# Kernel optimization log

Hardware: AMD Instinct MI355X
Metric: run time of the kernel (lower is better)

## Reference

```python
import jax, jax.numpy as jnp
import numpy as np
import math

D_MODEL = 1024
N_HEADS = 16
D_K = D_MODEL // N_HEADS


def setup_inputs() -> dict:
    key = jax.random.key(0)
    ks = jax.random.split(key, 5)
    std = math.sqrt(2.0 / (D_MODEL + D_MODEL))
    x = jax.random.normal(ks[0], (2, 2048, D_MODEL), dtype=jnp.float32)
    W_q = jax.random.normal(ks[1], (D_MODEL, D_MODEL), dtype=jnp.float32) * std
    W_k = jax.random.normal(ks[2], (D_MODEL, D_MODEL), dtype=jnp.float32) * std
    W_v = jax.random.normal(ks[3], (D_MODEL, D_MODEL), dtype=jnp.float32) * std
    W_o = jax.random.normal(ks[4], (D_MODEL, D_MODEL), dtype=jnp.float32) * std
    return {"x": x, "W_q": W_q, "W_k": W_k, "W_v": W_v, "W_o": W_o}


def reference(x, W_q, W_k, W_v, W_o):
    B, S, D = x.shape
    H, dk = N_HEADS, D_K
    # projections: (B,S,D) @ (D,D)
    def split_heads(t):  # (B,S,D) -> (B,H,S,dk)
        return t.reshape(B, S, H, dk).transpose(0, 2, 1, 3)
    Q = split_heads(x @ W_q)
    K = split_heads(x @ W_k)
    V = split_heads(x @ W_v)
    scale = 1.0 / math.sqrt(dk)
    scores = jnp.einsum("bhqd,bhkd->bhqk", Q, K) * scale  # (B,H,S,S)
    attn = jax.nn.softmax(scores, axis=-1)
    out = jnp.einsum("bhqk,bhkd->bhqd", attn, V)  # (B,H,S,dk)
    concat = out.transpose(0, 2, 1, 3).reshape(B, S, D)
    return concat @ W_o
```

## Files before the change

### kernel.cpp

```cpp
#include <hip/hip_runtime.h>
#include <hip/hip_bf16.h>
#include <math.h>

#define DMODEL 1024
#define NHEADS 16
#define DKH    64
#define BATCH  2
#define SEQ    2048
#define MROWS  (BATCH * SEQ)
#define LOG2E  1.4426950408889634f

typedef __bf16 bf16_t;
typedef bf16_t bf16x8 __attribute__((ext_vector_type(8)));
typedef bf16_t bf16x4 __attribute__((ext_vector_type(4)));
typedef float  floatx4 __attribute__((ext_vector_type(4)));

__device__ __forceinline__ void glds16(const bf16_t* g, bf16_t* l) {
    __builtin_amdgcn_global_load_lds((__attribute__((address_space(1))) unsigned*)(g),
                                     (__attribute__((address_space(3))) unsigned*)(l),
                                     16, 0, 0);
}

__global__ void prep_kernel(const float* __restrict__ x,
                            const float* __restrict__ W0, const float* __restrict__ W1,
                            const float* __restrict__ W2, const float* __restrict__ W3,
                            bf16_t* __restrict__ xb, bf16_t* __restrict__ Wt) {
    __shared__ float t[32][33];
    int bx = blockIdx.x, by = blockIdx.y, z = blockIdx.z;
    int tx = threadIdx.x, ty = threadIdx.y;
    if (z == 0) {
        int tid = ty * 32 + tx;
#pragma unroll
        for (int k = 0; k < 4; ++k) {
            int slot = k * 256 + tid;
            int row = by * 128 + (slot >> 3);
            int col = bx * 32 + (slot & 7) * 4;
            float4 v = *(const float4*)&x[(size_t)row * DMODEL + col];
            bf16x4 o = {(bf16_t)v.x, (bf16_t)v.y, (bf16_t)v.z, (bf16_t)v.w};
            *(bf16x4*)&xb[(size_t)row * DMODEL + col] = o;
        }
        return;
    }
    const float* W = (z == 1) ? W0 : (z == 2) ? W1 : (z == 3) ? W2 : W3;
    bf16_t* dst = Wt + (size_t)(z - 1) * DMODEL * DMODEL;
#pragma unroll
    for (int i = 0; i < 32; i += 8)
        t[ty + i][tx] = W[(size_t)(by * 32 + ty + i) * DMODEL + bx * 32 + tx];
    __syncthreads();
#pragma unroll
    for (int i = 0; i < 32; i += 8)
        dst[(size_t)(bx * 32 + ty + i) * DMODEL + by * 32 + tx] = (bf16_t)t[tx][ty + i];
}

__global__ __launch_bounds__(512) void gemm_qkv_kernel(const bf16_t* __restrict__ A,
                                                       const bf16_t* __restrict__ Bt,
                                                       bf16_t* __restrict__ Qfb,
                                                       bf16_t* __restrict__ Kfb,
                                                       bf16_t* __restrict__ Vfb) {
    extern __shared__ __align__(16) bf16_t sm[];
    int tid = threadIdx.x;
    int w = tid >> 6, l = tid & 63, g = l >> 4, lm = l & 15;
    int wr = w >> 2, wc = w & 3;
    int m0 = blockIdx.y * 256, n0 = blockIdx.x * 256;

    int w8l3 = w * 8 + (l >> 3);
    int cw8  = ((l & 7) ^ (l >> 3)) * 8;
    const bf16_t* Ag0 = A  + (size_t)m0 * DMODEL;
    const bf16_t* Bg0 = Bt + (size_t)n0 * DMODEL;

#define STAGE(MATB, LDSB, hh, tt) do {                                             \
        const bf16_t* _src = (MATB) + (size_t)((hh) * 128 + w8l3) * DMODEL + (tt) * 64 + cw8; \
        bf16_t* _dst = (LDSB) + (hh) * 8192 + w * 8 * 64;                          \
        glds16(_src, _dst);                                                        \
        glds16(_src + (size_t)64 * DMODEL, _dst + 4096);                           \
    } while (0)

#define PH_SYNC() do { asm volatile("s_waitcnt vmcnt(4)" ::: "memory");            \
        __builtin_amdgcn_s_barrier(); __builtin_amdgcn_sched_barrier(0); } while (0)
#define PH_BAR() do { __builtin_amdgcn_s_barrier();                                \
        __builtin_amdgcn_sched_barrier(0); } while (0)

    floatx4 a00[4][2], a01[4][2], a10[4][2], a11[4][2];
#pragma unroll
    for (int i = 0; i < 4; ++i)
#pragma unroll
        for (int j = 0; j < 2; ++j) {
            floatx4 z = {0.f, 0.f, 0.f, 0.f};
            a00[i][j] = z; a01[i][j] = z; a10[i][j] = z; a11[i][j] = z;
        }
    bf16x8 af[4][2], bf0[2][2], bf1[2][2];

#define LOAD_AF(ihh, bb) do {                                                      \
        const bf16_t* _ab = sm + (bb) * 16384 + (ihh) * 8192;                      \
        _Pragma("unroll")                                                          \
        for (int i = 0; i < 4; ++i) {                                              \
            int _hr = (wr * 64 + i * 16 + lm) * 64;                                \
            af[i][0] = *(const bf16x8*)&_ab[_hr + ((g) ^ (lm & 7)) * 8];           \
            af[i][1] = *(const bf16x8*)&_ab[_hr + ((4 + g) ^ (lm & 7)) * 8];       \
        } } while (0)

#define LOAD_BF(BF, jhh, bb) do {                                                  \
        const bf16_t* _bb = sm + 32768 + (bb) * 16384 + (jhh) * 8192;              \
        _Pragma("unroll")                                                          \
        for (int j = 0; j < 2; ++j) {                                              \
            int _bc = (wc * 32 + j * 16 + lm) * 64;                                \
            BF[j][0] = *(const bf16x8*)&_bb[_bc + ((g) ^ (lm & 7)) * 8];           \
            BF[j][1] = *(const bf16x8*)&_bb[_bc + ((4 + g) ^ (lm & 7)) * 8];       \
        } } while (0)

#define MM(ACC, BF) do {                                                           \
        __builtin_amdgcn_s_setprio(1);                                             \
        _Pragma("unroll")                                                          \
        for (int kk = 0; kk < 2; ++kk)                                             \
        _Pragma("unroll")                                                          \
        for (int i = 0; i < 4; ++i)                                                \
        _Pragma("unroll")                                                          \
        for (int j = 0; j < 2; ++j)                                                \
            ACC[i][j] = __builtin_amdgcn_mfma_f32_16x16x32_bf16(af[i][kk], BF[j][kk], ACC[i][j], 0, 0, 0); \
        __builtin_amdgcn_s_setprio(0);                                             \
    } while (0)

    STAGE(Ag0, sm, 0, 0);
    STAGE(Bg0, sm + 32768, 0, 0);
    STAGE(Bg0, sm + 32768, 1, 0);
    STAGE(Ag0, sm, 1, 0);

    for (int t = 0; t < 16; ++t) {
        int buf = t & 1;
        bf16_t* An = sm + (buf ^ 1) * 16384;
        bf16_t* Bn = sm + 32768 + (buf ^ 1) * 16384;
        int tn = (t + 1) & 15;

        PH_SYNC();
        STAGE(Ag0, An, 0, tn);
        LOAD_AF(0, buf);
        LOAD_BF(bf0, 0, buf);
        MM(a00, bf0);
        PH_SYNC();
        STAGE(Bg0, Bn, 0, tn);
        LOAD_BF(bf1, 1, buf);
        MM(a01, bf1);
        PH_SYNC();
        STAGE(Bg0, Bn, 1, tn);
        LOAD_AF(1, buf);
        MM(a11, bf1);
        PH_BAR();
        STAGE(Ag0, An, 1, tn);
        MM(a10, bf0);
    }

    __syncthreads();
    int mat = blockIdx.x >> 2;
    int headb = (blockIdx.x & 3) * 4;
    int b = m0 >> 11;
    int ktb = (m0 & 2047) >> 6;
    const float scaleQ = 0.125f * LOG2E;

#define EPI(ACC, ihh, jhh)                                                          \
    _Pragma("unroll")                                                               \
    for (int i = 0; i < 4; ++i)                                                     \
    _Pragma("unroll")                                                               \
    for (int j = 0; j < 2; ++j) {                                                   \
        int s0_ = (ihh) * 128 + wr * 64 + i * 16 + g * 4;                           \
        int d_  = (jhh) * 128 + wc * 32 + j * 16 + lm;                              \
        int hc_ = d_ >> 6, d6 = d_ & 63, st_ = s0_ >> 6, s6 = s0_ & 63;             \
        int chunk = hc_ * 4 + st_;                                                  \
        if (mat == 0) {                                                             \
            int base = chunk * 4096 + ((s6 >> 4) * 2 + (d6 >> 5)) * 512 +           \
                       ((d6 >> 3) & 3) * 128 + (s6 & 15) * 8 + (d6 & 7);            \
            _Pragma("unroll")                                                       \
            for (int r = 0; r < 4; ++r)                                             \
                sm[base + r * 8] = (bf16_t)(ACC[i][j][r] * scaleQ);                 \
        } else if (mat == 1) {                                                      \
            int base = chunk * 4096 + (((s6 >> 5) & 1) * 4 + ((s6 >> 2) & 1) * 2 + (d6 >> 5)) * 512 + \
                       ((d6 >> 3) & 3) * 128 +                                      \
                       (((s6 >> 4) & 1) * 8 + ((s6 >> 3) & 1) * 4) * 8 + (d6 & 7);  \
            _Pragma("unroll")                                                       \
            for (int r = 0; r < 4; ++r)                                             \
                sm[base + r * 8] = (bf16_t)ACC[i][j][r];                            \
        } else {                                                                    \
            int base = chunk * 4096 + ((d6 >> 4) * 2 + ((s6 >> 5) & 1)) * 512 +     \
                       ((((s6 >> 4) & 1) * 2 + ((s6 >> 3) & 1)) * 16 + (d6 & 15)) * 8 + \
                       ((s6 >> 2) & 1) * 4;                                         \
            bf16x4 pk = {(bf16_t)ACC[i][j][0], (bf16_t)ACC[i][j][1],                \
                         (bf16_t)ACC[i][j][2], (bf16_t)ACC[i][j][3]};               \
            *(bf16x4*)&sm[base] = pk;                                               \
        }                                                                           \
    }

    EPI(a00, 0, 0);
    EPI(a01, 0, 1);
    EPI(a10, 1, 0);
    EPI(a11, 1, 1);

    __syncthreads();
    bf16_t* outbuf = (mat == 0) ? Qfb : (mat == 1) ? Kfb : Vfb;
#pragma unroll
    for (int rep = 0; rep < 16; ++rep) {
        int idx = rep * 512 + tid;
        int c = idx >> 9;
        int off = (idx & 511) * 8;
        int bh2 = b * NHEADS + headb + (c >> 2);
        int kt = ktb + (c & 3);
        *(bf16x8*)(outbuf + ((size_t)bh2 * 32 + kt) * 4096 + off) = *(const bf16x8*)&sm[c * 4096 + off];
    }
#undef STAGE
#undef PH_SYNC
#undef PH_BAR
#undef LOAD_AF
#undef LOAD_BF
#undef MM
#undef EPI
}

__global__ __launch_bounds__(256) void gemmO_kernel(const bf16_t* __restrict__ A,
                                                    const bf16_t* __restrict__ Bt,
                                                    float* __restrict__ outp) {
    __shared__ bf16_t As[64 * 64];
    __shared__ bf16_t Bs[128 * 64];
    int tid = threadIdx.x;
    int w = tid >> 6, l = tid & 63, g = l >> 4, lm = l & 15;
    int wr = w & 1, wc = w >> 1;
    int m0 = blockIdx.y * 64, n0 = blockIdx.x * 128;
    int r8 = l >> 3, s8 = l & 7, cw = s8 ^ r8;

    floatx4 acc[2][4];
#pragma unroll
    for (int i = 0; i < 2; ++i)
#pragma unroll
        for (int j = 0; j < 4; ++j) { floatx4 z = {0.f, 0.f, 0.f, 0.f}; acc[i][j] = z; }

    const bf16_t* Ag = A  + (size_t)(m0 + w * 16 + r8) * DMODEL + cw * 8;
    const bf16_t* Bg = Bt + (size_t)(n0 + w * 32 + r8) * DMODEL + cw * 8;

    for (int k0 = 0; k0 < DMODEL; k0 += 64) {
        __syncthreads();
#pragma unroll
        for (int j = 0; j < 2; ++j)
            glds16(Ag + (size_t)j * 8 * DMODEL + k0, &As[(w * 16 + j * 8) * 64]);
#pragma unroll
        for (int j = 0; j < 4; ++j)
            glds16(Bg + (size_t)j * 8 * DMODEL + k0, &Bs[(w * 32 + j * 8) * 64]);
        __syncthreads();
#pragma unroll
        for (int kk = 0; kk < 2; ++kk) {
            bf16x8 af[2], bfr[4];
            int c = kk * 4 + g;
            int sw = (c ^ (lm & 7)) * 8;
#pragma unroll
            for (int i = 0; i < 2; ++i)
                af[i] = *(const bf16x8*)&As[(wr * 32 + i * 16 + lm) * 64 + sw];
#pragma unroll
            for (int j = 0; j < 4; ++j)
                bfr[j] = *(const bf16x8*)&Bs[(wc * 64 + j * 16 + lm) * 64 + sw];
#pragma unroll
            for (int i = 0; i < 2; ++i)
#pragma unroll
                for (int j = 0; j < 4; ++j)
                    acc[i][j] = __builtin_amdgcn_mfma_f32_16x16x32_bf16(af[i], bfr[j], acc[i][j], 0, 0, 0);
        }
    }

#pragma unroll
    for (int i = 0; i < 2; ++i)
#pragma unroll
        for (int j = 0; j < 4; ++j) {
            int nc = n0 + wc * 64 + j * 16 + lm;
            int mb = m0 + wr * 32 + i * 16 + g * 4;
#pragma unroll
            for (int r = 0; r < 4; ++r)
                outp[(size_t)(mb + r) * DMODEL + nc] = acc[i][j][r];
        }
}

__global__ __launch_bounds__(256, 2) void attn_kernel(const bf16_t* __restrict__ Qf,
                                                      const bf16_t* __restrict__ Kf,
                                                      const bf16_t* __restrict__ Vf,
                                                      bf16_t* __restrict__ Cc) {
    __shared__ __align__(16) char smem[24576];
    float*  Mbuf = (float*)smem;
    float*  Lbuf = (float*)(smem + 20480);
    bf16_t* Ct   = (bf16_t*)(smem + 21504);

    int tid = threadIdx.x;
    int w = tid >> 6, l = tid & 63, g = l >> 4, lm = l & 15;
    int bh = blockIdx.x, b = bh >> 4, h = bh & 15;
    int q0 = blockIdx.y * 64;

    const bf16_t* Qfh = Qf + ((size_t)bh * 32 + (q0 >> 6)) * 4096 + l * 8;
    const bf16_t* Kfh = Kf + (size_t)bh * 32 * 4096 + l * 8;
    const bf16_t* Vfh = Vf + (size_t)bh * 32 * 4096 + l * 8;

    bf16x8 qf[4][2];
#pragma unroll
    for (int nt = 0; nt < 4; ++nt)
#pragma unroll
        for (int kk = 0; kk < 2; ++kk)
            qf[nt][kk] = *(const bf16x8*)(Qfh + (nt * 2 + kk) * 512);

    floatx4 oacc[4][4];
#pragma unroll
    for (int dt = 0; dt < 4; ++dt)
#pragma unroll
        for (int nt = 0; nt < 4; ++nt) { floatx4 z = {0.f, 0.f, 0.f, 0.f}; oacc[dt][nt] = z; }
    float lsum[4] = {0.f, 0.f, 0.f, 0.f};

    int kt0 = w * 8;
    bf16x8 kfa[2][2], kfb[2][2], vfa[4], vfb[4];
    {
        const bf16_t* Kb0 = Kfh + (size_t)kt0 * 4096;
#pragma unroll
        for (int c = 0; c < 2; ++c)
#pragma unroll
            for (int kk = 0; kk < 2; ++kk)
                kfa[c][kk] = *(const bf16x8*)(Kb0 + (c * 2 + kk) * 512);
    }

    for (int it = 0; it < 8; ++it) {
        const bf16_t* Tb = Kfh + (size_t)(kt0 + it) * 4096;
        const bf16_t* Vb = Vfh + (size_t)(kt0 + it) * 4096;
        const bf16_t* Tn = Kfh + (size_t)(kt0 + ((it < 7) ? it + 1 : 0)) * 4096;

#pragma unroll
        for (int dt = 0; dt < 4; ++dt) vfa[dt] = *(const bf16x8*)(Vb + (dt * 2 + 0) * 512);
#pragma unroll
        for (int c = 0; c < 2; ++c)
#pragma unroll
            for (int kk = 0; kk < 2; ++kk)
                kfb[c][kk] = *(const bf16x8*)(Tb + (4 + c * 2 + kk) * 512);

        floatx4 sa[2][4];
#pragma unroll
        for (int c = 0; c < 2; ++c)
#pragma unroll
            for (int nt = 0; nt < 4; ++nt) { floatx4 z = {0.f, 0.f, 0.f, 0.f}; sa[c][nt] = z; }
        __builtin_amdgcn_s_setprio(1);
#pragma unroll
        for (int kk = 0; kk < 2; ++kk)
#pragma unroll
            for (int c = 0; c < 2; ++c)
#pragma unroll
                for (int nt = 0; nt < 4; ++nt)
                    sa[c][nt] = __builtin_amdgcn_mfma_f32_16x16x32_bf16(kfa[c][kk], qf[nt][kk], sa[c][nt], 0, 0, 0);
        __builtin_amdgcn_s_setprio(0);

#pragma unroll
        for (int dt = 0; dt < 4; ++dt) vfb[dt] = *(const bf16x8*)(Vb + (dt * 2 + 1) * 512);
#pragma unroll
        for (int c = 0; c < 2; ++c)
#pragma unroll
            for (int kk = 0; kk < 2; ++kk)
                kfa[c][kk] = *(const bf16x8*)(Tn + (c * 2 + kk) * 512);

        floatx4 sb[2][4];
#pragma unroll
        for (int c = 0; c < 2; ++c)
#pragma unroll
            for (int nt = 0; nt < 4; ++nt) { floatx4 z = {0.f, 0.f, 0.f, 0.f}; sb[c][nt] = z; }
        __builtin_amdgcn_s_setprio(1);
#pragma unroll
        for (int kk = 0; kk < 2; ++kk)
#pragma unroll
            for (int c = 0; c < 2; ++c)
#pragma unroll
                for (int nt = 0; nt < 4; ++nt)
                    sb[c][nt] = __builtin_amdgcn_mfma_f32_16x16x32_bf16(kfb[c][kk], qf[nt][kk], sb[c][nt], 0, 0, 0);
        __builtin_amdgcn_s_setprio(0);

        {
            bf16x8 bp[4];
#pragma unroll
            for (int nt = 0; nt < 4; ++nt) {
                float p0 = __builtin_amdgcn_exp2f(sa[0][nt][0]);
                float p1 = __builtin_amdgcn_exp2f(sa[0][nt][1]);
                float p2 = __builtin_amdgcn_exp2f(sa[0][nt][2]);
                float p3 = __builtin_amdgcn_exp2f(sa[0][nt][3]);
                float p4 = __builtin_amdgcn_exp2f(sa[1][nt][0]);
                float p5 = __builtin_amdgcn_exp2f(sa[1][nt][1]);
                float p6 = __builtin_amdgcn_exp2f(sa[1][nt][2]);
                float p7 = __builtin_amdgcn_exp2f(sa[1][nt][3]);
                lsum[nt] += ((p0 + p1) + (p2 + p3)) + ((p4 + p5) + (p6 + p7));
                bf16x8 pk = {(bf16_t)p0, (bf16_t)p1, (bf16_t)p2, (bf16_t)p3,
                             (bf16_t)p4, (bf16_t)p5, (bf16_t)p6, (bf16_t)p7};
                bp[nt] = pk;
            }
            __builtin_amdgcn_s_setprio(1);
#pragma unroll
            for (int dt = 0; dt < 4; ++dt)
#pragma unroll
                for (int nt = 0; nt < 4; ++nt)
                    oacc[dt][nt] = __builtin_amdgcn_mfma_f32_16x16x32_bf16(vfa[dt], bp[nt], oacc[dt][nt], 0, 0, 0);
            __builtin_amdgcn_s_setprio(0);
        }

        {
            bf16x8 bp[4];
#pragma unroll
            for (int nt = 0; nt < 4; ++nt) {
                float p0 = __builtin_amdgcn_exp2f(sb[0][nt][0]);
                float p1 = __builtin_amdgcn_exp2f(sb[0][nt][1]);
                float p2 = __builtin_amdgcn_exp2f(sb[0][nt][2]);
                float p3 = __builtin_amdgcn_exp2f(sb[0][nt][3]);
                float p4 = __builtin_amdgcn_exp2f(sb[1][nt][0]);
                float p5 = __builtin_amdgcn_exp2f(sb[1][nt][1]);
                float p6 = __builtin_amdgcn_exp2f(sb[1][nt][2]);
                float p7 = __builtin_amdgcn_exp2f(sb[1][nt][3]);
                lsum[nt] += ((p0 + p1) + (p2 + p3)) + ((p4 + p5) + (p6 + p7));
                bf16x8 pk = {(bf16_t)p0, (bf16_t)p1, (bf16_t)p2, (bf16_t)p3,
                             (bf16_t)p4, (bf16_t)p5, (bf16_t)p6, (bf16_t)p7};
                bp[nt] = pk;
            }
            __builtin_amdgcn_s_setprio(1);
#pragma unroll
            for (int dt = 0; dt < 4; ++dt)
#pragma unroll
                for (int nt = 0; nt < 4; ++nt)
                    oacc[dt][nt] = __builtin_amdgcn_mfma_f32_16x16x32_bf16(vfb[dt], bp[nt], oacc[dt][nt], 0, 0, 0);
            __builtin_amdgcn_s_setprio(0);
        }
    }

#pragma unroll
    for (int nt = 0; nt < 4; ++nt) {
        float s = lsum[nt];
        s += __shfl_xor(s, 16, 64);
        s += __shfl_xor(s, 32, 64);
        lsum[nt] = s;
    }

    float linv = 0.f;
#pragma unroll
    for (int p = 0; p < 4; ++p) {
        __syncthreads();
#pragma unroll
        for (int nt = 0; nt < 4; ++nt)
            *(floatx4*)&Mbuf[w * 1280 + (nt * 16 + lm) * 20 + g * 4] = oacc[p][nt];
        if (p == 0 && g == 0)
#pragma unroll
            for (int nt = 0; nt < 4; ++nt)
                Lbuf[w * 64 + nt * 16 + lm] = lsum[nt];
        __syncthreads();
        if (p == 0) {
            float lt = 0.f;
#pragma unroll
            for (int w2 = 0; w2 < 4; ++w2)
                lt += Lbuf[w2 * 64 + w * 16 + lm];
            linv = 1.0f / lt;
        }
        {
            floatx4 s = {0.f, 0.f, 0.f, 0.f};
#pragma unroll
            for (int w2 = 0; w2 < 4; ++w2)
                s += *(const floatx4*)&Mbuf[w2 * 1280 + (w * 16 + lm) * 20 + g * 4];
            bf16x4 pk = {(bf16_t)(s[0] * linv), (bf16_t)(s[1] * linv),
                         (bf16_t)(s[2] * linv), (bf16_t)(s[3] * linv)};
            *(bf16x4*)&Ct[w * 384 + lm * 24 + g * 4] = pk;
        }
        {
            int row = l >> 2, dp = l & 3;
            bf16x4 v = *(const bf16x4*)&Ct[w * 384 + row * 24 + dp * 4];
            *(bf16x4*)&Cc[((size_t)(b * SEQ + q0 + w * 16 + row)) * DMODEL + h * DKH + p * 16 + dp * 4] = v;
        }
    }
}

extern "C" void kernel_launch(void* const* d_in, const int* in_sizes, int n_in,
                              void* d_out, int out_size, void* d_ws, size_t ws_size,
                              hipStream_t stream) {
    const float* x  = (const float*)d_in[0];
    const float* Wq = (const float*)d_in[1];
    const float* Wk = (const float*)d_in[2];
    const float* Wv = (const float*)d_in[3];
    const float* Wo = (const float*)d_in[4];

    const size_t NX = (size_t)MROWS * DMODEL;
    const size_t NW = (size_t)DMODEL * DMODEL;
    bf16_t* ws  = (bf16_t*)d_ws;
    bf16_t* xb  = ws;
    bf16_t* Wt  = xb + NX;
    bf16_t* Wto = Wt + 3 * NW;
    bf16_t* Qfb = Wt + 4 * NW;
    bf16_t* Kfb = Qfb + NX;
    bf16_t* Vfb = Kfb + NX;
    bf16_t* Cc  = Vfb + NX;

    prep_kernel<<<dim3(32, 32, 5), dim3(32, 8), 0, stream>>>(x, Wq, Wk, Wv, Wo, xb, Wt);

    gemm_qkv_kernel<<<dim3(12, 16), 512, 131072, stream>>>(xb, Wt, Qfb, Kfb, Vfb);

    attn_kernel<<<dim3(BATCH * NHEADS, SEQ / 64), 256, 0, stream>>>(Qfb, Kfb, Vfb, Cc);

    gemmO_kernel<<<dim3(DMODEL / 128, MROWS / 64), 256, 0, stream>>>(Cc, Wto, (float*)d_out);
}
```

Before: 165.9 us.

## Stage K/V through double-buffered LDS in attention and enlarge output-GEMM tiles

Result: slower. 181.2 us (+9.2%).

```diff
diff --git a/kernel.cpp b/kernel.cpp
--- a/kernel.cpp
+++ b/kernel.cpp
@@ -216,45 +216,43 @@
 __global__ __launch_bounds__(256) void gemmO_kernel(const bf16_t* __restrict__ A,
                                                     const bf16_t* __restrict__ Bt,
                                                     float* __restrict__ outp) {
-    __shared__ bf16_t As[64 * 64];
+    __shared__ bf16_t As[128 * 64];
     __shared__ bf16_t Bs[128 * 64];
     int tid = threadIdx.x;
     int w = tid >> 6, l = tid & 63, g = l >> 4, lm = l & 15;
-    int wr = w & 1, wc = w >> 1;
-    int m0 = blockIdx.y * 64, n0 = blockIdx.x * 128;
+    int wr = w >> 1, wc = w & 1;
+    int m0 = blockIdx.y * 128, n0 = blockIdx.x * 128;
     int r8 = l >> 3, s8 = l & 7, cw = s8 ^ r8;
 
-    floatx4 acc[2][4];
-#pragma unroll
-    for (int i = 0; i < 2; ++i)
+    floatx4 acc[4][4];
+#pragma unroll
+    for (int i = 0; i < 4; ++i)
 #pragma unroll
         for (int j = 0; j < 4; ++j) { floatx4 z = {0.f, 0.f, 0.f, 0.f}; acc[i][j] = z; }
 
-    const bf16_t* Ag = A  + (size_t)(m0 + w * 16 + r8) * DMODEL + cw * 8;
+    const bf16_t* Ag = A  + (size_t)(m0 + w * 32 + r8) * DMODEL + cw * 8;
     const bf16_t* Bg = Bt + (size_t)(n0 + w * 32 + r8) * DMODEL + cw * 8;
 
     for (int k0 = 0; k0 < DMODEL; k0 += 64) {
         __syncthreads();
 #pragma unroll
-        for (int j = 0; j < 2; ++j)
-            glds16(Ag + (size_t)j * 8 * DMODEL + k0, &As[(w * 16 + j * 8) * 64]);
-#pragma unroll
-        for (int j = 0; j < 4; ++j)
+        for (int j = 0; j < 4; ++j) {
+            glds16(Ag + (size_t)j * 8 * DMODEL + k0, &As[(w * 32 + j * 8) * 64]);
             glds16(Bg + (size_t)j * 8 * DMODEL + k0, &Bs[(w * 32 + j * 8) * 64]);
+        }
         __syncthreads();
 #pragma unroll
         for (int kk = 0; kk < 2; ++kk) {
-            bf16x8 af[2], bfr[4];
+            bf16x8 af[4], bfr[4];
             int c = kk * 4 + g;
             int sw = (c ^ (lm & 7)) * 8;
 #pragma unroll
-            for (int i = 0; i < 2; ++i)
-                af[i] = *(const bf16x8*)&As[(wr * 32 + i * 16 + lm) * 64 + sw];
-#pragma unroll
-            for (int j = 0; j < 4; ++j)
-                bfr[j] = *(const bf16x8*)&Bs[(wc * 64 + j * 16 + lm) * 64 + sw];
-#pragma unroll
-            for (int i = 0; i < 2; ++i)
+            for (int i = 0; i < 4; ++i) {
+                af[i]  = *(const bf16x8*)&As[(wr * 64 + i * 16 + lm) * 64 + sw];
+                bfr[i] = *(const bf16x8*)&Bs[(wc * 64 + i * 16 + lm) * 64 + sw];
+            }
+#pragma unroll
+            for (int i = 0; i < 4; ++i)
 #pragma unroll
                 for (int j = 0; j < 4; ++j)
                     acc[i][j] = __builtin_amdgcn_mfma_f32_16x16x32_bf16(af[i], bfr[j], acc[i][j], 0, 0, 0);
@@ -262,25 +260,22 @@
     }
 
 #pragma unroll
-    for (int i = 0; i < 2; ++i)
+    for (int i = 0; i < 4; ++i)
 #pragma unroll
         for (int j = 0; j < 4; ++j) {
             int nc = n0 + wc * 64 + j * 16 + lm;
-            int mb = m0 + wr * 32 + i * 16 + g * 4;
+            int mb = m0 + wr * 64 + i * 16 + g * 4;
 #pragma unroll
             for (int r = 0; r < 4; ++r)
                 outp[(size_t)(mb + r) * DMODEL + nc] = acc[i][j][r];
         }
 }
 
-__global__ __launch_bounds__(256, 2) void attn_kernel(const bf16_t* __restrict__ Qf,
-                                                      const bf16_t* __restrict__ Kf,
-                                                      const bf16_t* __restrict__ Vf,
-                                                      bf16_t* __restrict__ Cc) {
-    __shared__ __align__(16) char smem[24576];
-    float*  Mbuf = (float*)smem;
-    float*  Lbuf = (float*)(smem + 20480);
-    bf16_t* Ct   = (bf16_t*)(smem + 21504);
+__global__ __launch_bounds__(256) void attn_kernel(const bf16_t* __restrict__ Qf,
+                                                   const bf16_t* __restrict__ Kf,
+                                                   const bf16_t* __restrict__ Vf,
+                                                   bf16_t* __restrict__ Cc) {
+    __shared__ __align__(16) bf16_t kv[2][8192];
 
     int tid = threadIdx.x;
     int w = tid >> 6, l = tid & 63, g = l >> 4, lm = l & 15;
@@ -288,179 +283,139 @@
     int q0 = blockIdx.y * 64;
 
     const bf16_t* Qfh = Qf + ((size_t)bh * 32 + (q0 >> 6)) * 4096 + l * 8;
-    const bf16_t* Kfh = Kf + (size_t)bh * 32 * 4096 + l * 8;
-    const bf16_t* Vfh = Vf + (size_t)bh * 32 * 4096 + l * 8;
-
-    bf16x8 qf[4][2];
-#pragma unroll
-    for (int nt = 0; nt < 4; ++nt)
+    const bf16_t* Kg  = Kf + (size_t)bh * 32 * 4096;
+    const bf16_t* Vg  = Vf + (size_t)bh * 32 * 4096;
+
+    bf16x8 qf[2];
+    qf[0] = *(const bf16x8*)(Qfh + (w * 2 + 0) * 512);
+    qf[1] = *(const bf16x8*)(Qfh + (w * 2 + 1) * 512);
+
+    floatx4 oacc[4];
+#pragma unroll
+    for (int dt = 0; dt < 4; ++dt) { floatx4 z = {0.f, 0.f, 0.f, 0.f}; oacc[dt] = z; }
+    float lsum = 0.f;
+
+#define AST(bb, kt) do {                                                           \
+        const bf16_t* _k = Kg + (size_t)(kt) * 4096 + w * 512 + l * 8;             \
+        const bf16_t* _v = Vg + (size_t)(kt) * 4096 + w * 512 + l * 8;             \
+        bf16_t* _dk = &kv[bb][w * 512];                                            \
+        bf16_t* _dv = &kv[bb][4096 + w * 512];                                     \
+        glds16(_k, _dk);                                                           \
+        glds16(_k + 2048, _dk + 2048);                                             \
+        glds16(_v, _dv);                                                           \
+        glds16(_v + 2048, _dv + 2048);                                             \
+    } while (0)
+
+    AST(0, 0);
+    __syncthreads();
+
+    for (int t = 0; t < 32; ++t) {
+        int cur = t & 1;
+        if (t < 31) AST(cur ^ 1, t + 1);
+        const bf16_t* Kb = &kv[cur][0] + l * 8;
+        const bf16_t* Vb = &kv[cur][4096] + l * 8;
+
+        bf16x8 kf[2][2];
+#pragma unroll
+        for (int c = 0; c < 2; ++c)
+#pragma unroll
+            for (int kk = 0; kk < 2; ++kk)
+                kf[c][kk] = *(const bf16x8*)(Kb + (c * 2 + kk) * 512);
+        floatx4 sa[2];
+#pragma unroll
+        for (int c = 0; c < 2; ++c) { floatx4 z = {0.f, 0.f, 0.f, 0.f}; sa[c] = z; }
+        __builtin_amdgcn_s_setprio(1);
 #pragma unroll
         for (int kk = 0; kk < 2; ++kk)
-            qf[nt][kk] = *(const bf16x8*)(Qfh + (nt * 2 + kk) * 512);
-
-    floatx4 oacc[4][4];
-#pragma unroll
-    for (int dt = 0; dt < 4; ++dt)
-#pragma unroll
-        for (int nt = 0; nt < 4; ++nt) { floatx4 z = {0.f, 0.f, 0.f, 0.f}; oacc[dt][nt] = z; }
-    float lsum[4] = {0.f, 0.f, 0.f, 0.f};
-
-    int kt0 = w * 8;
-    bf16x8 kfa[2][2], kfb[2][2], vfa[4], vfb[4];
-    {
-        const bf16_t* Kb0 = Kfh + (size_t)kt0 * 4096;
+#pragma unroll
+            for (int c = 0; c < 2; ++c)
+                sa[c] = __builtin_amdgcn_mfma_f32_16x16x32_bf16(kf[c][kk], qf[kk], sa[c], 0, 0, 0);
+        __builtin_amdgcn_s_setprio(0);
+
+        bf16x8 kf2[2][2];
 #pragma unroll
         for (int c = 0; c < 2; ++c)
 #pragma unroll
             for (int kk = 0; kk < 2; ++kk)
-                kfa[c][kk] = *(const bf16x8*)(Kb0 + (c * 2 + kk) * 512);
-    }
-
-    for (int it = 0; it < 8; ++it) {
-        const bf16_t* Tb = Kfh + (size_t)(kt0 + it) * 4096;
-        const bf16_t* Vb = Vfh + (size_t)(kt0 + it) * 4096;
-        const bf16_t* Tn = Kfh + (size_t)(kt0 + ((it < 7) ? it + 1 : 0)) * 4096;
-
-#pragma unroll
-        for (int dt = 0; dt < 4; ++dt) vfa[dt] = *(const bf16x8*)(Vb + (dt * 2 + 0) * 512);
-#pragma unroll
-        for (int c = 0; c < 2; ++c)
-#pragma unroll
-            for (int kk = 0; kk < 2; ++kk)
-                kfb[c][kk] = *(const bf16x8*)(Tb + (4 + c * 2 + kk) * 512);
-
-        floatx4 sa[2][4];
-#pragma unroll
-        for (int c = 0; c < 2; ++c)
-#pragma unroll
-            for (int nt = 0; nt < 4; ++nt) { floatx4 z = {0.f, 0.f, 0.f, 0.f}; sa[c][nt] = z; }
+                kf2[c][kk] = *(const bf16x8*)(Kb + (4 + c * 2 + kk) * 512);
+        floatx4 sb[2];
+#pragma unroll
+        for (int c = 0; c < 2; ++c) { floatx4 z = {0.f, 0.f, 0.f, 0.f}; sb[c] = z; }
         __builtin_amdgcn_s_setprio(1);
 #pragma unroll
         for (int kk = 0; kk < 2; ++kk)
 #pragma unroll
             for (int c = 0; c < 2; ++c)
-#pragma unroll
-                for (int nt = 0; nt < 4; ++nt)
-                    sa[c][nt] = __builtin_amdgcn_mfma_f32_16x16x32_bf16(kfa[c][kk], qf[nt][kk], sa[c][nt], 0, 0, 0);
+                sb[c] = __builtin_amdgcn_mfma_f32_16x16x32_bf16(kf2[c][kk], qf[kk], sb[c], 0, 0, 0);
         __builtin_amdgcn_s_setprio(0);
 
-#pragma unroll
-        for (int dt = 0; dt < 4; ++dt) vfb[dt] = *(const bf16x8*)(Vb + (dt * 2 + 1) * 512);
-#pragma unroll
-        for (int c = 0; c < 2; ++c)
-#pragma unroll
-            for (int kk = 0; kk < 2; ++kk)
-                kfa[c][kk] = *(const bf16x8*)(Tn + (c * 2 + kk) * 512);
-
-        floatx4 sb[2][4];
-#pragma unroll
-        for (int c = 0; c < 2; ++c)
-#pragma unroll
-            for (int nt = 0; nt < 4; ++nt) { floatx4 z = {0.f, 0.f, 0.f, 0.f}; sb[c][nt] = z; }
-        __builtin_amdgcn_s_setprio(1);
-#pragma unroll
-        for (int kk = 0; kk < 2; ++kk)
-#pragma unroll
-            for (int c = 0; c < 2; ++c)
-#pragma unroll
-                for (int nt = 0; nt < 4; ++nt)
-                    sb[c][nt] = __builtin_amdgcn_mfma_f32_16x16x32_bf16(kfb[c][kk], qf[nt][kk], sb[c][nt], 0, 0, 0);
-        __builtin_amdgcn_s_setprio(0);
-
         {
-            bf16x8 bp[4];
-#pragma unroll
-            for (int nt = 0; nt < 4; ++nt) {
-                float p0 = __builtin_amdgcn_exp2f(sa[0][nt][0]);
-                float p1 = __builtin_amdgcn_exp2f(sa[0][nt][1]);
-                float p2 = __builtin_amdgcn_exp2f(sa[0][nt][2]);
-                float p3 = __builtin_amdgcn_exp2f(sa[0][nt][3]);
-                float p4 = __builtin_amdgcn_exp2f(sa[1][nt][0]);
-                float p5 = __builtin_amdgcn_exp2f(sa[1][nt][1]);
-                float p6 = __builtin_amdgcn_exp2f(sa[1][nt][2]);
-                float p7 = __builtin_amdgcn_exp2f(sa[1][nt][3]);
-                lsum[nt] += ((p0 + p1) + (p2 + p3)) + ((p4 + p5) + (p6 + p7));
-                bf16x8 pk = {(bf16_t)p0, (bf16_t)p1, (bf16_t)p2, (bf16_t)p3,
-                             (bf16_t)p4, (bf16_t)p5, (bf16_t)p6, (bf16_t)p7};
-                bp[nt] = pk;
-            }
+            float p0 = __builtin_amdgcn_exp2f(sa[0][0]);
+            float p1 = __builtin_amdgcn_exp2f(sa[0][1]);
+            float p2 = __builtin_amdgcn_exp2f(sa[0][2]);
+            float p3 = __builtin_amdgcn_exp2f(sa[0][3]);
+            float p4 = __builtin_amdgcn_exp2f(sa[1][0]);
+            float p5 = __builtin_amdgcn_exp2f(sa[1][1]);
+            float p6 = __builtin_amdgcn_exp2f(sa[1][2]);
+            float p7 = __builtin_amdgcn_exp2f(sa[1][3]);
+            lsum += ((p0 + p1) + (p2 + p3)) + ((p4 + p5) + (p6 + p7));
+            bf16x8 bp = {(bf16_t)p0, (bf16_t)p1, (bf16_t)p2, (bf16_t)p3,
+                         (bf16_t)p4, (bf16_t)p5, (bf16_t)p6, (bf16_t)p7};
+            bf16x8 vf[4];
+#pragma unroll
+            for (int dt = 0; dt < 4; ++dt)
+                vf[dt] = *(const bf16x8*)(Vb + (dt * 2 + 0) * 512);
             __builtin_amdgcn_s_setprio(1);
 #pragma unroll
             for (int dt = 0; dt < 4; ++dt)
-#pragma unroll
-                for (int nt = 0; nt < 4; ++nt)
-                    oacc[dt][nt] = __builtin_amdgcn_mfma_f32_16x16x32_bf16(vfa[dt], bp[nt], oacc[dt][nt], 0, 0, 0);
+                oacc[dt] = __builtin_amdgcn_mfma_f32_16x16x32_bf16(vf[dt], bp, oacc[dt], 0, 0, 0);
             __builtin_amdgcn_s_setprio(0);
         }
-
         {
-            bf16x8 bp[4];
-#pragma unroll
-            for (int nt = 0; nt < 4; ++nt) {
-                float p0 = __builtin_amdgcn_exp2f(sb[0][nt][0]);
-                float p1 = __builtin_amdgcn_exp2f(sb[0][nt][1]);
-                float p2 = __builtin_amdgcn_exp2f(sb[0][nt][2]);
-                float p3 = __builtin_amdgcn_exp2f(sb[0][nt][3]);
-                float p4 = __builtin_amdgcn_exp2f(sb[1][nt][0]);
-                float p5 = __builtin_amdgcn_exp2f(sb[1][nt][1]);
-                float p6 = __builtin_amdgcn_exp2f(sb[1][nt][2]);
-                float p7 = __builtin_amdgcn_exp2f(sb[1][nt][3]);
-                lsum[nt] += ((p0 + p1) + (p2 + p3)) + ((p4 + p5) + (p6 + p7));
-                bf16x8 pk = {(bf16_t)p0, (bf16_t)p1, (bf16_t)p2, (bf16_t)p3,
-                             (bf16_t)p4, (bf16_t)p5, (bf16_t)p6, (bf16_t)p7};
-                bp[nt] = pk;
-            }
+            float p0 = __builtin_amdgcn_exp2f(sb[0][0]);
+            float p1 = __builtin_amdgcn_exp2f(sb[0][1]);
+            float p2 = __builtin_amdgcn_exp2f(sb[0][2]);
+            float p3 = __builtin_amdgcn_exp2f(sb[0][3]);
+            float p4 = __builtin_amdgcn_exp2f(sb[1][0]);
+            float p5 = __builtin_amdgcn_exp2f(sb[1][1]);
+            float p6 = __builtin_amdgcn_exp2f(sb[1][2]);
+            float p7 = __builtin_amdgcn_exp2f(sb[1][3]);
+            lsum += ((p0 + p1) + (p2 + p3)) + ((p4 + p5) + (p6 + p7));
+            bf16x8 bp = {(bf16_t)p0, (bf16_t)p1, (bf16_t)p2, (bf16_t)p3,
+                         (bf16_t)p4, (bf16_t)p5, (bf16_t)p6, (bf16_t)p7};
+            bf16x8 vf[4];
+#pragma unroll
+            for (int dt = 0; dt < 4; ++dt)
+                vf[dt] = *(const bf16x8*)(Vb + (dt * 2 + 1) * 512);
             __builtin_amdgcn_s_setprio(1);
 #pragma unroll
             for (int dt = 0; dt < 4; ++dt)
-#pragma unroll
-                for (int nt = 0; nt < 4; ++nt)
-                    oacc[dt][nt] = __builtin_amdgcn_mfma_f32_16x16x32_bf16(vfb[dt], bp[nt], oacc[dt][nt], 0, 0, 0);
+                oacc[dt] = __builtin_amdgcn_mfma_f32_16x16x32_bf16(vf[dt], bp, oacc[dt], 0, 0, 0);
             __builtin_amdgcn_s_setprio(0);
         }
-    }
-
-#pragma unroll
-    for (int nt = 0; nt < 4; ++nt) {
-        float s = lsum[nt];
-        s += __shfl_xor(s, 16, 64);
-        s += __shfl_xor(s, 32, 64);
-        lsum[nt] = s;
-    }
-
-    float linv = 0.f;
-#pragma unroll
-    for (int p = 0; p < 4; ++p) {
+
         __syncthreads();
-#pragma unroll
-        for (int nt = 0; nt < 4; ++nt)
-            *(floatx4*)&Mbuf[w * 1280 + (nt * 16 + lm) * 20 + g * 4] = oacc[p][nt];
-        if (p == 0 && g == 0)
-#pragma unroll
-            for (int nt = 0; nt < 4; ++nt)
-                Lbuf[w * 64 + nt * 16 + lm] = lsum[nt];
-        __syncthreads();
-        if (p == 0) {
-            float lt = 0.f;
-#pragma unroll
-            for (int w2 = 0; w2 < 4; ++w2)
-                lt += Lbuf[w2 * 64 + w * 16 + lm];
-            linv = 1.0f / lt;
-        }
-        {
-            floatx4 s = {0.f, 0.f, 0.f, 0.f};
-#pragma unroll
-            for (int w2 = 0; w2 < 4; ++w2)
-                s += *(const floatx4*)&Mbuf[w2 * 1280 + (w * 16 + lm) * 20 + g * 4];
-            bf16x4 pk = {(bf16_t)(s[0] * linv), (bf16_t)(s[1] * linv),
-                         (bf16_t)(s[2] * linv), (bf16_t)(s[3] * linv)};
-            *(bf16x4*)&Ct[w * 384 + lm * 24 + g * 4] = pk;
-        }
-        {
-            int row = l >> 2, dp = l & 3;
-            bf16x4 v = *(const bf16x4*)&Ct[w * 384 + row * 24 + dp * 4];
-            *(bf16x4*)&Cc[((size_t)(b * SEQ + q0 + w * 16 + row)) * DMODEL + h * DKH + p * 16 + dp * 4] = v;
-        }
+    }
+#undef AST
+
+    lsum += __shfl_xor(lsum, 16, 64);
+    lsum += __shfl_xor(lsum, 32, 64);
+    float linv = 1.0f / lsum;
+
+    bf16_t* Ct = (bf16_t*)kv;
+#pragma unroll
+    for (int dt = 0; dt < 4; ++dt) {
+        bf16x4 pk = {(bf16_t)(oacc[dt][0] * linv), (bf16_t)(oacc[dt][1] * linv),
+                     (bf16_t)(oacc[dt][2] * linv), (bf16_t)(oacc[dt][3] * linv)};
+        *(bf16x4*)&Ct[w * 1152 + lm * 72 + dt * 16 + g * 4] = pk;
+    }
+    asm volatile("s_waitcnt lgkmcnt(0)" ::: "memory");
+    __builtin_amdgcn_sched_barrier(0);
+#pragma unroll
+    for (int p = 0; p < 2; ++p) {
+        int row = p * 8 + (l >> 3), ch = l & 7;
+        bf16x8 v = *(const bf16x8*)&Ct[w * 1152 + row * 72 + ch * 8];
+        *(bf16x8*)&Cc[((size_t)(b * SEQ + q0 + w * 16 + row)) * DMODEL + h * DKH + ch * 8] = v;
     }
 }
 
@@ -490,5 +445,5 @@
 
     attn_kernel<<<dim3(BATCH * NHEADS, SEQ / 64), 256, 0, stream>>>(Qfb, Kfb, Vfb, Cc);
 
-    gemmO_kernel<<<dim3(DMODEL / 128, MROWS / 64), 256, 0, stream>>>(Cc, Wto, (float*)d_out);
-}
+    gemmO_kernel<<<dim3(DMODEL / 128, MROWS / 128), 256, 0, stream>>>(Cc, Wto, (float*)d_out);
+}
```
